# Kernel optimization log

Hardware: AMD Instinct MI355X
Metric: run time of the kernel (lower is better)

## Reference

```python
import jax, jax.numpy as jnp
import numpy as np

B, N = 8, 2048
EPS = 0.01

def setup_inputs() -> dict:
    key = jax.random.key(0)
    k_w, k_p, k_t = jax.random.split(key, 3)
    # W[:, 1] is the adjacency channel; entries are 0/1 floats
    W = jax.random.randint(k_w, (B, 2, N, N), 0, 2).astype(jnp.float32)
    pred = jax.random.normal(k_p, (B, N), dtype=jnp.float32)
    tgt = jax.random.randint(k_t, (B, N), 0, 16)  # unused by the loss, kept for signature fidelity
    return {"W": W, "pred": pred, "tgt": tgt}

def reference(W, pred, tgt):
    # adjacency mask from channel 1: [B, N, N]
    adj = W[:, 1] == 1.0
    # pairwise |pred_i - pred_j| < eps: [B, N, N]
    close = jnp.abs(pred[:, :, None] - pred[:, None, :]) < EPS
    # count of conflicting (same-color) adjacent pairs, returned as shape (1,) like torch mark
    mark = jnp.sum(jnp.where(adj & close, 1.0, 0.0), dtype=jnp.float32)
    return mark.reshape(1)
```

## Files before the change

kernel.cpp:

```cpp
#include <hip/hip_runtime.h>

#define BB 8
#define NN 2048
#define EPS 0.01f
#define ROWS 8
#define BLOCKS_PER_B 256
#define NBLK (BB * BLOCKS_PER_B)

__global__ __launch_bounds__(256, 4) void coloring_loss_stage1(
    const float* __restrict__ W,
    const float* __restrict__ pred,
    float* __restrict__ partial)
{
    __shared__ float s_partial[4];

    const int bid  = blockIdx.x;
    const int b    = bid >> 8;
    const int row0 = (bid & 255) * ROWS;
    const int t    = threadIdx.x;

    const float* predb = pred + (size_t)b * NN;

    const float4 pj0 = ((const float4*)predb)[t];
    const float4 pj1 = ((const float4*)predb)[t + 256];

    float pis[ROWS];
#pragma unroll
    for (int r = 0; r < ROWS; ++r) pis[r] = predb[row0 + r];

    const float* wbase = W + (((size_t)b * 2 + 1) * (size_t)NN + (size_t)row0) * (size_t)NN;

    int cnt = 0;
#pragma unroll
    for (int r = 0; r < ROWS; ++r) {
        const float4* w4 = (const float4*)(wbase + (size_t)r * NN);
        const float4 w0 = w4[t];
        const float4 w1 = w4[t + 256];
        const float pi = pis[r];
        cnt += (w0.x == 1.0f) && (fabsf(pi - pj0.x) < EPS);
        cnt += (w0.y == 1.0f) && (fabsf(pi - pj0.y) < EPS);
        cnt += (w0.z == 1.0f) && (fabsf(pi - pj0.z) < EPS);
        cnt += (w0.w == 1.0f) && (fabsf(pi - pj0.w) < EPS);
        cnt += (w1.x == 1.0f) && (fabsf(pi - pj1.x) < EPS);
        cnt += (w1.y == 1.0f) && (fabsf(pi - pj1.y) < EPS);
        cnt += (w1.z == 1.0f) && (fabsf(pi - pj1.z) < EPS);
        cnt += (w1.w == 1.0f) && (fabsf(pi - pj1.w) < EPS);
    }

#pragma unroll
    for (int off = 32; off > 0; off >>= 1)
        cnt += __shfl_down(cnt, off, 64);

    const int wave = t >> 6;
    const int lane = t & 63;
    if (lane == 0) s_partial[wave] = (float)cnt;
    __syncthreads();

    if (t == 0) {
        partial[bid] = s_partial[0] + s_partial[1] + s_partial[2] + s_partial[3];
    }
}

__global__ __launch_bounds__(256) void coloring_loss_stage2(
    const float* __restrict__ partial,
    float* __restrict__ out)
{
    __shared__ float s_partial[4];
    const int t = threadIdx.x;

    float s = 0.0f;
#pragma unroll
    for (int k = 0; k < NBLK / 256; ++k)
        s += partial[t + k * 256];

#pragma unroll
    for (int off = 32; off > 0; off >>= 1)
        s += __shfl_down(s, off, 64);

    const int wave = t >> 6;
    const int lane = t & 63;
    if (lane == 0) s_partial[wave] = s;
    __syncthreads();

    if (t == 0)
        out[0] = s_partial[0] + s_partial[1] + s_partial[2] + s_partial[3];
}

extern "C" void kernel_launch(void* const* d_in, const int* in_sizes, int n_in,
                              void* d_out, int out_size, void* d_ws, size_t ws_size,
                              hipStream_t stream) {
    const float* W    = (const float*)d_in[0];
    const float* pred = (const float*)d_in[1];
    float* out     = (float*)d_out;
    float* partial = (float*)d_ws;

    coloring_loss_stage1<<<NBLK, 256, 0, stream>>>(W, pred, partial);
    coloring_loss_stage2<<<1, 256, 0, stream>>>(partial, out);
}
```

Before: 322.2 us.

## Use fewer blocks with software-prefetched row loop and nontemporal loads

Reduces the grid to 512 blocks that each process 32 rows, loading the next W row while the current row is compared, and uses nontemporal loads for the streaming adjacency data. The intent is to amortise per-block setup and overlap loads with compute while avoiding cache pollution. In exchange it reduces the number of loads in flight per thread and the number of resident waves, which may lower memory-level parallelism.

```diff
diff --git a/kernel.cpp b/kernel.cpp
--- a/kernel.cpp
+++ b/kernel.cpp
@@ -1,42 +1,49 @@
 #include <hip/hip_runtime.h>
 
-#define BB 8
 #define NN 2048
 #define EPS 0.01f
-#define ROWS 8
-#define BLOCKS_PER_B 256
-#define NBLK (BB * BLOCKS_PER_B)
+#define NBLK 512
+#define ROWS_PB 32
+#define BLK_PER_B 64
 
-__global__ __launch_bounds__(256, 4) void coloring_loss_stage1(
+typedef float vfloat4 __attribute__((ext_vector_type(4)));
+
+__global__ __launch_bounds__(256) void coloring_loss_stage1(
     const float* __restrict__ W,
     const float* __restrict__ pred,
     float* __restrict__ partial)
 {
     __shared__ float s_partial[4];
 
-    const int bid  = blockIdx.x;
-    const int b    = bid >> 8;
-    const int row0 = (bid & 255) * ROWS;
-    const int t    = threadIdx.x;
+    const int bid = blockIdx.x;
+    const int b   = bid / BLK_PER_B;
+    const int i0  = (bid % BLK_PER_B) * ROWS_PB;
+    const int t   = threadIdx.x;
 
     const float* predb = pred + (size_t)b * NN;
 
-    const float4 pj0 = ((const float4*)predb)[t];
-    const float4 pj1 = ((const float4*)predb)[t + 256];
+    const vfloat4 pj0 = ((const vfloat4*)predb)[t];
+    const vfloat4 pj1 = ((const vfloat4*)predb)[t + 256];
 
-    float pis[ROWS];
-#pragma unroll
-    for (int r = 0; r < ROWS; ++r) pis[r] = predb[row0 + r];
+    const float* wbase = W + (((size_t)b * 2 + 1) * (size_t)NN + (size_t)i0) * (size_t)NN;
 
-    const float* wbase = W + (((size_t)b * 2 + 1) * (size_t)NN + (size_t)row0) * (size_t)NN;
+    const vfloat4* w4 = (const vfloat4*)wbase;
+    vfloat4 w0 = __builtin_nontemporal_load(&w4[t]);
+    vfloat4 w1 = __builtin_nontemporal_load(&w4[t + 256]);
 
     int cnt = 0;
-#pragma unroll
-    for (int r = 0; r < ROWS; ++r) {
-        const float4* w4 = (const float4*)(wbase + (size_t)r * NN);
-        const float4 w0 = w4[t];
-        const float4 w1 = w4[t + 256];
-        const float pi = pis[r];
+    for (int r = 0; r < ROWS_PB; ++r) {
+        vfloat4 nw0, nw1;
+        if (r + 1 < ROWS_PB) {
+            const vfloat4* n4 = (const vfloat4*)(wbase + (size_t)(r + 1) * (size_t)NN);
+            nw0 = __builtin_nontemporal_load(&n4[t]);
+            nw1 = __builtin_nontemporal_load(&n4[t + 256]);
+        } else {
+            nw0 = w0; nw1 = w1;
+        }
+
+        const float pi = predb[i0 + r];
+
         cnt += (w0.x == 1.0f) && (fabsf(pi - pj0.x) < EPS);
         cnt += (w0.y == 1.0f) && (fabsf(pi - pj0.y) < EPS);
         cnt += (w0.z == 1.0f) && (fabsf(pi - pj0.z) < EPS);
@@ -45,6 +52,8 @@
         cnt += (w1.y == 1.0f) && (fabsf(pi - pj1.y) < EPS);
         cnt += (w1.z == 1.0f) && (fabsf(pi - pj1.z) < EPS);
         cnt += (w1.w == 1.0f) && (fabsf(pi - pj1.w) < EPS);
+
+        w0 = nw0; w1 = nw1;
     }
 
 #pragma unroll
@@ -56,9 +65,8 @@
     if (lane == 0) s_partial[wave] = (float)cnt;
     __syncthreads();
 
-    if (t == 0) {
+    if (t == 0)
         partial[bid] = s_partial[0] + s_partial[1] + s_partial[2] + s_partial[3];
-    }
 }
 
 __global__ __launch_bounds__(256) void coloring_loss_stage2(
@@ -68,10 +76,7 @@
     __shared__ float s_partial[4];
     const int t = threadIdx.x;
 
-    float s = 0.0f;
-#pragma unroll
-    for (int k = 0; k < NBLK / 256; ++k)
-        s += partial[t + k * 256];
+    float s = partial[t] + partial[t + 256];
 
 #pragma unroll
     for (int off = 32; off > 0; off >>= 1)
```

New measurement: 322.6 us, median of 2. About the same (+0.1%).
